# Optimization experiments

Measured on AMD Instinct MI355X. Metric: run time of the kernel, lower is better.

Reference implementation:

```python
import jax, jax.numpy as jnp
import numpy as np

T = 8192   # sequence length (sent_len)
D = 512    # word_emb_dim
H = 2048   # enc_lstm_dim
S = 512    # number of segments (len(action_pos))
EPS = 1e-4 # additive constant in the original _masked_softmax denominator


def setup_inputs() -> dict:
    key = jax.random.key(0)
    ks = jax.random.split(key, 16)
    s = 0.02  # small init scale keeps exp() stable
    seg_len = T // S
    action_pos = (jnp.arange(1, S + 1, dtype=jnp.int32) * seg_len - 1)  # last = T-1
    action = jnp.zeros((T,), jnp.int32).at[action_pos].set(1)
    return {
        "sent": jax.random.normal(ks[0], (T, D), jnp.float32),
        "Wi1": jax.random.normal(ks[1], (3 * H, D), jnp.float32) * s,
        "Wh1": jax.random.normal(ks[2], (3 * H, H), jnp.float32) * s,
        "bi1": jax.random.normal(ks[3], (3 * H,), jnp.float32) * s,
        "bh1": jax.random.normal(ks[4], (3 * H,), jnp.float32) * s,
        "Wi2": jax.random.normal(ks[5], (3 * H, H), jnp.float32) * s,
        "Wh2": jax.random.normal(ks[6], (3 * H, H), jnp.float32) * s,
        "bi2": jax.random.normal(ks[7], (3 * H,), jnp.float32) * s,
        "bh2": jax.random.normal(ks[8], (3 * H,), jnp.float32) * s,
        "Wl": jax.random.normal(ks[9], (H, H), jnp.float32) * s,
        "bl": jax.random.normal(ks[10], (H,), jnp.float32) * s,
        "wa": jax.random.normal(ks[11], (H,), jnp.float32) * s,
        "Wl2": jax.random.normal(ks[12], (H, H), jnp.float32) * s,
        "bl2": jax.random.normal(ks[13], (H,), jnp.float32) * s,
        "wa2": jax.random.normal(ks[14], (H,), jnp.float32) * s,
        "action": action,
        "action_pos": action_pos,
    }


def _gru_scan(xs, reset, Wi, Wh, bi, bh):
    """GRU over leading axis; hidden state zeroed after steps where reset==1.
    xs: (N, in), reset: (N,) int. Returns outputs (N, H)."""
    gi_all = xs @ Wi.T + bi  # (N, 3H) precompute input gates as one GEMM

    def step(h, inp):
        gi, a = inp
        gh = Wh @ h + bh
        r = jax.nn.sigmoid(gi[:H] + gh[:H])
        z = jax.nn.sigmoid(gi[H:2 * H] + gh[H:2 * H])
        n = jnp.tanh(gi[2 * H:] + r * gh[2 * H:])
        hn = (1.0 - z) * n + z * h
        h_next = jnp.where(a == 1, jnp.zeros_like(hn), hn)
        return h_next, hn

    h0 = jnp.zeros((H,), xs.dtype)
    _, outs = jax.lax.scan(step, h0, (gi_all, reset))
    return outs


def _degenerate_softmax(a):
    # Original sums exp over a size-1 axis: w = exp(a) / (exp(a) + 1e-4)
    e = jnp.exp(a)
    return e / (e + EPS)


def reference(sent, Wi1, Wh1, bi1, bh1, Wi2, Wh2, bi2, bh2,
              Wl, bl, wa, Wl2, bl2, wa2, action, action_pos):
    # lower GRU with per-step state reset
    outs = _gru_scan(sent, action, Wi1, Wh1, bi1, bh1)          # (T, H)
    emb_h = jnp.tanh(outs @ Wl.T + bl)                           # (T, H)
    w = _degenerate_softmax(emb_h @ wa)                          # (T,)
    weighted = w[:, None] * emb_h                                # (T, H)
    # segment i covers tokens (action_pos[i-1], action_pos[i]]
    seg_id = jnp.searchsorted(action_pos, jnp.arange(T), side='left')
    seg = jax.ops.segment_max(weighted, seg_id, num_segments=S)  # (S, H)
    # upper GRU over segment embeddings (no resets, zero init)
    outs2 = _gru_scan(seg, jnp.zeros((S,), jnp.int32), Wi2, Wh2, bi2, bh2)
    e2 = jnp.tanh(outs2 @ Wl2.T + bl2)                           # (S, H)
    w2 = _degenerate_softmax(e2 @ wa2)                           # (S,)
    emb = jnp.max(w2[:, None] * e2, axis=0, keepdims=True)       # (1, H)
    return emb
```

## Files before the change

### kernel.cpp

```cpp
#include <hip/hip_runtime.h>
#include <stdint.h>

typedef unsigned short u16;
typedef unsigned int u32;
typedef unsigned long long u64;
typedef __attribute__((ext_vector_type(4))) float f32x4;
typedef __attribute__((ext_vector_type(8))) short bf16x8;
typedef __attribute__((ext_vector_type(4))) u32 u32x4;

constexpr int kT = 8192;
constexpr int kD = 512;
constexpr int kH = 2048;
constexpr int kH3 = 6144;
constexpr int kS = 512;
constexpr int kSeg = 16;
constexpr int kNWG2 = 256;
constexpr int kREP = 4;

__device__ __forceinline__ float bf2f(u16 u) {
  union { float f; u32 u; } v; v.u = ((u32)u) << 16; return v.f;
}
__device__ __forceinline__ u16 f2bf(float f) {
  union { float f; u32 u; } v; v.f = f;
  u32 lsb = (v.u >> 16) & 1u;
  v.u += 0x7fffu + lsb;
  return (u16)(v.u >> 16);
}
__device__ __forceinline__ float bflo(u32 x) {
  union { float f; u32 u; } v; v.u = x << 16; return v.f;
}
__device__ __forceinline__ float bfhi(u32 x) {
  union { float f; u32 u; } v; v.u = x & 0xffff0000u; return v.f;
}
__device__ __forceinline__ float sigm(float x) { return 1.f / (1.f + expf(-x)); }

__device__ __forceinline__ void g2l16(const u16* g, u16* l) {
  __builtin_amdgcn_global_load_lds(
      (const __attribute__((address_space(1))) u32*)g,
      (__attribute__((address_space(3))) u32*)l, 16, 0, 0);
}

__device__ __forceinline__ u32x4 bypass_load16(const u32* p) {
  u32x4 v;
  asm volatile("global_load_dwordx4 %0, %1, off sc0 sc1\n\ts_waitcnt vmcnt(0)"
               : "=&v"(v) : "v"(p) : "memory");
  return v;
}
__device__ __forceinline__ void bypass_store4(u32* p, u32 v) {
  asm volatile("global_store_dword %0, %1, off sc0 sc1" :: "v"(p), "v"(v) : "memory");
}

struct Cvt7 {
  const float* s[7];
  u16* d[7];
  u32 pref[8];
};
__global__ __launch_bounds__(256) void cvt_all(Cvt7 j, int n4tot) {
  int i = blockIdx.x * 256 + threadIdx.x;
  if (i >= n4tot) return;
  int r = 0;
  while (i >= (int)j.pref[r + 1]) ++r;
  const int local = i - (int)j.pref[r];
  const float4 v = ((const float4*)j.s[r])[local];
  uint2 o;
  o.x = (u32)f2bf(v.x) | ((u32)f2bf(v.y) << 16);
  o.y = (u32)f2bf(v.z) | ((u32)f2bf(v.w) << 16);
  ((uint2*)j.d[r])[local] = o;
}

template<int EPI>
__global__ __launch_bounds__(256)
void gemm_bt(const u16* __restrict__ A, int lda,
             const u16* __restrict__ B, int ldb,
             u16* __restrict__ Obf, const float* __restrict__ bias,
             int M, int N, int K)
{
  __shared__ u16 ls[4 * 16384];
  const int tid = threadIdx.x;
  const int w = tid >> 6, lane = tid & 63;
  const int wr = w >> 1, wc = w & 1;
  const int arow0 = blockIdx.y * 128;
  const int brow0 = blockIdx.x * 128;
  const int srow = w * 32 + (lane >> 3);
  const int scol = (lane & 7) * 8;
  const u16* gA = A + (size_t)(arow0 + srow) * lda + scol;
  const u16* gB = B + (size_t)(brow0 + srow) * ldb + scol;
  const int sb = w * 32 * 64;

  f32x4 acc[4][4];
#pragma unroll
  for (int m = 0; m < 4; ++m)
#pragma unroll
    for (int n = 0; n < 4; ++n) acc[m][n] = (f32x4)0.f;

  const int fr = lane & 15;
  const int kq = lane >> 4;
  const int nk = K >> 6;

  auto stage = [&](int buf, int kt) {
    u16* la = &ls[buf * 16384 + sb];
    u16* lb = &ls[buf * 16384 + 8192 + sb];
#pragma unroll
    for (int i = 0; i < 4; ++i) g2l16(gA + (size_t)i * 8 * lda + kt, la + i * 8 * 64);
#pragma unroll
    for (int i = 0; i < 4; ++i) g2l16(gB + (size_t)i * 8 * ldb + kt, lb + i * 8 * 64);
  };

  stage(0, 0);
  if (nk > 1) stage(1, 64);
  if (nk > 2) stage(2, 128);

  for (int i = 0; i < nk; ++i) {
    if (i + 2 < nk) asm volatile("s_waitcnt vmcnt(16)" ::: "memory");
    else            asm volatile("s_waitcnt vmcnt(0)" ::: "memory");
    __builtin_amdgcn_s_barrier();
    __builtin_amdgcn_sched_barrier(0);
    if (i + 3 < nk) stage((i + 3) & 3, (i + 3) * 64);
    const u16* lsA = &ls[(i & 3) * 16384];
    const u16* lsB = lsA + 8192;
#pragma unroll
    for (int kk = 0; kk < 2; ++kk) {
      bf16x8 af[4], bq[4];
#pragma unroll
      for (int m = 0; m < 4; ++m)
        af[m] = *(const bf16x8*)&lsA[(wr * 64 + m * 16 + fr) * 64 + kk * 32 + kq * 8];
#pragma unroll
      for (int n = 0; n < 4; ++n)
        bq[n] = *(const bf16x8*)&lsB[(wc * 64 + n * 16 + fr) * 64 + kk * 32 + kq * 8];
#pragma unroll
      for (int m = 0; m < 4; ++m)
#pragma unroll
        for (int n = 0; n < 4; ++n)
          acc[m][n] = __builtin_amdgcn_mfma_f32_16x16x32_bf16(af[m], bq[n], acc[m][n], 0, 0, 0);
    }
  }

#pragma unroll
  for (int m = 0; m < 4; ++m) {
#pragma unroll
    for (int n = 0; n < 4; ++n) {
      const int row0 = arow0 + wr * 64 + m * 16 + kq * 4;
      const int col = brow0 + wc * 64 + n * 16 + fr;
      if (EPI == 1) {
#pragma unroll
        for (int i = 0; i < 4; ++i)
          Obf[(size_t)(row0 + i) * N + col] = f2bf(acc[m][n][i]);
      } else {
        const float bv = bias[col];
#pragma unroll
        for (int i = 0; i < 4; ++i)
          Obf[(size_t)(row0 + i) * N + col] = f2bf(tanhf(acc[m][n][i] + bv));
      }
    }
  }
}

template<int EPI>
__global__ __launch_bounds__(256)
void gemm_bt64(const u16* __restrict__ A, int lda,
               const u16* __restrict__ B, int ldb,
               u16* __restrict__ Obf, const float* __restrict__ bias,
               int M, int N, int K)
{
  __shared__ u16 ls[4 * 8192];
  const int tid = threadIdx.x;
  const int w = tid >> 6, lane = tid & 63;
  const int wr = w >> 1, wc = w & 1;
  const int arow0 = blockIdx.y * 64;
  const int brow0 = blockIdx.x * 64;
  const int srow = w * 16 + (lane >> 3);
  const int scol = (lane & 7) * 8;
  const u16* gA = A + (size_t)(arow0 + srow) * lda + scol;
  const u16* gB = B + (size_t)(brow0 + srow) * ldb + scol;
  const int sb = w * 16 * 64;

  f32x4 acc[2][2];
#pragma unroll
  for (int m = 0; m < 2; ++m)
#pragma unroll
    for (int n = 0; n < 2; ++n) acc[m][n] = (f32x4)0.f;

  const int fr = lane & 15;
  const int kq = lane >> 4;
  const int nk = K >> 6;

  auto stage = [&](int buf, int kt) {
    u16* la = &ls[buf * 8192 + sb];
    u16* lb = &ls[buf * 8192 + 4096 + sb];
#pragma unroll
    for (int i = 0; i < 2; ++i) g2l16(gA + (size_t)i * 8 * lda + kt, la + i * 8 * 64);
#pragma unroll
    for (int i = 0; i < 2; ++i) g2l16(gB + (size_t)i * 8 * ldb + kt, lb + i * 8 * 64);
  };

  stage(0, 0);
  if (nk > 1) stage(1, 64);
  if (nk > 2) stage(2, 128);

  for (int i = 0; i < nk; ++i) {
    if (i + 2 < nk) asm volatile("s_waitcnt vmcnt(8)" ::: "memory");
    else            asm volatile("s_waitcnt vmcnt(0)" ::: "memory");
    __builtin_amdgcn_s_barrier();
    __builtin_amdgcn_sched_barrier(0);
    if (i + 3 < nk) stage((i + 3) & 3, (i + 3) * 64);
    const u16* lsA = &ls[(i & 3) * 8192];
    const u16* lsB = lsA + 4096;
#pragma unroll
    for (int kk = 0; kk < 2; ++kk) {
      bf16x8 af[2], bq[2];
#pragma unroll
      for (int m = 0; m < 2; ++m)
        af[m] = *(const bf16x8*)&lsA[(wr * 32 + m * 16 + fr) * 64 + kk * 32 + kq * 8];
#pragma unroll
      for (int n = 0; n < 2; ++n)
        bq[n] = *(const bf16x8*)&lsB[(wc * 32 + n * 16 + fr) * 64 + kk * 32 + kq * 8];
#pragma unroll
      for (int m = 0; m < 2; ++m)
#pragma unroll
        for (int n = 0; n < 2; ++n)
          acc[m][n] = __builtin_amdgcn_mfma_f32_16x16x32_bf16(af[m], bq[n], acc[m][n], 0, 0, 0);
    }
  }

#pragma unroll
  for (int m = 0; m < 2; ++m) {
#pragma unroll
    for (int n = 0; n < 2; ++n) {
      const int row0 = arow0 + wr * 32 + m * 16 + kq * 4;
      const int col = brow0 + wc * 32 + n * 16 + fr;
      if (EPI == 1) {
#pragma unroll
        for (int i = 0; i < 4; ++i)
          Obf[(size_t)(row0 + i) * N + col] = f2bf(acc[m][n][i]);
      } else {
        const float bv = bias[col];
#pragma unroll
        for (int i = 0; i < 4; ++i)
          Obf[(size_t)(row0 + i) * N + col] = f2bf(tanhf(acc[m][n][i] + bv));
      }
    }
  }
}

__global__ __launch_bounds__(256) void gru1_gates(
    const u32* __restrict__ gi32, int segStride, const u16* __restrict__ gh,
    const float* __restrict__ bi, const float* __restrict__ bh,
    u16* __restrict__ h_bf, u16* __restrict__ outs_bf, int t, int ghvalid)
{
  const int idx = blockIdx.x * 256 + threadIdx.x;
  const int seg = idx >> 10, jp = idx & 1023;
  const u32* gh32 = (const u32*)gh;
  const int gbase = seg * segStride;
  const int base = seg * 3072;
  const u32 gir = gi32[gbase + jp];
  const u32 giz = gi32[gbase + 1024 + jp];
  const u32 gin = gi32[gbase + 2048 + jp];
  u32 ghr = 0, ghz = 0, ghn = 0, hp = 0;
  if (ghvalid) {
    ghr = gh32[base + jp];
    ghz = gh32[base + 1024 + jp];
    ghn = gh32[base + 2048 + jp];
    hp = ((const u32*)h_bf)[seg * 1024 + jp];
  }
  const float2 bir = *(const float2*)&bi[2 * jp];
  const float2 biz = *(const float2*)&bi[kH + 2 * jp];
  const float2 bin = *(const float2*)&bi[2 * kH + 2 * jp];
  const float2 bhr = *(const float2*)&bh[2 * jp];
  const float2 bhz = *(const float2*)&bh[kH + 2 * jp];
  const float2 bhn = *(const float2*)&bh[2 * kH + 2 * jp];
  float hn[2];
#pragma unroll
  for (int e = 0; e < 2; ++e) {
    const float gr = e ? bfhi(gir) : bflo(gir), hr = e ? bfhi(ghr) : bflo(ghr);
    const float gz = e ? bfhi(giz) : bflo(giz), hz = e ? bfhi(ghz) : bflo(ghz);
    const float gn = e ? bfhi(gin) : bflo(gin), hh = e ? bfhi(ghn) : bflo(ghn);
    const float r = sigm(gr + (e ? bir.y : bir.x) + hr + (e ? bhr.y : bhr.x));
    const float z = sigm(gz + (e ? biz.y : biz.x) + hz + (e ? bhz.y : bhz.x));
    const float n = tanhf(gn + (e ? bin.y : bin.x) + r * (hh + (e ? bhn.y : bhn.x)));
    const float hprev = e ? bfhi(hp) : bflo(hp);
    hn[e] = (1.f - z) * n + z * hprev;
  }
  const u32 packed = (u32)f2bf(hn[0]) | ((u32)f2bf(hn[1]) << 16);
  ((u32*)h_bf)[seg * 1024 + jp] = packed;
  ((u32*)outs_bf)[(size_t)(seg * kSeg + t) * 1024 + jp] = packed;
}

__global__ __launch_bounds__(256) void seg_weight_max(
    const u16* __restrict__ embh, const float* __restrict__ wa,
    u16* __restrict__ seg_bf)
{
  __shared__ float wrow[16];
  const int s = blockIdx.x, tid = threadIdx.x;
  const int w = tid >> 6, lane = tid & 63;
#pragma unroll
  for (int rr = 0; rr < 4; ++rr) {
    const int r = w * 4 + rr;
    const u16* row = embh + ((size_t)s * kSeg + r) * kH;
    float p = 0.f;
#pragma unroll
    for (int k = 0; k < 32; ++k) {
      const int c = lane + 64 * k;
      p += bf2f(row[c]) * wa[c];
    }
#pragma unroll
    for (int off = 32; off; off >>= 1) p += __shfl_down(p, off, 64);
    if (lane == 0) { const float e = expf(p); wrow[r] = e / (e + 1e-4f); }
  }
  __syncthreads();
#pragma unroll
  for (int i = 0; i < 8; ++i) {
    const int c = tid + 256 * i;
    float m = -1e30f;
#pragma unroll
    for (int r = 0; r < 16; ++r)
      m = fmaxf(m, wrow[r] * bf2f(embh[((size_t)s * kSeg + r) * kH + c]));
    seg_bf[(size_t)s * kH + c] = f2bf(m);
  }
}

__global__ __launch_bounds__(512)
void gru2_persistent(const u16* __restrict__ Wh2bf, const u16* __restrict__ gi2b,
                     const float* __restrict__ bi2, const float* __restrict__ bh2,
                     u32* __restrict__ hx,
                     u16* __restrict__ outs2)
{
  __shared__ u32 hlb[2][1024];
  __shared__ float gil_all[512 * 24];
  __shared__ u32 hnlt[8];
  const int wg = blockIdx.x, tid = threadIdx.x;
  const int g0 = wg * 8;
  const int rep = wg & (kREP - 1);
  const int w = tid >> 6, lane = tid & 63;
  const int jj = g0 + w;

  u32 wr_[16], wz_[16], wn_[16];
  {
    const u32* rr = (const u32*)(Wh2bf + (size_t)jj * kH);
    const u32* rz = (const u32*)(Wh2bf + (size_t)(kH + jj) * kH);
    const u32* rn = (const u32*)(Wh2bf + (size_t)(2 * kH + jj) * kH);
#pragma unroll
    for (int q = 0; q < 4; ++q)
#pragma unroll
      for (int i = 0; i < 4; ++i) {
        const int idx = q * 256 + lane * 4 + i;
        wr_[q * 4 + i] = rr[idx];
        wz_[q * 4 + i] = rz[idx];
        wn_[q * 4 + i] = rn[idx];
      }
  }
  for (int i = tid; i < 512 * 24; i += 512) {
    const int t = i / 24, idx = i - t * 24;
    gil_all[i] = bf2f(gi2b[(size_t)t * kH3 + (idx >> 3) * kH + g0 + (idx & 7)]);
  }
  const float bir = bi2[jj], biz = bi2[kH + jj], bin = bi2[2 * kH + jj];
  const float bhr = bh2[jj], bhz = bh2[kH + jj], bhn = bh2[2 * kH + jj];
  if (tid < 8) hnlt[tid] = 0;
  __syncthreads();

  for (int t = 0; t < 512; ++t) {
    const int par = t & 1;
    const u32 want = (u32)t & 0xffffu;
    const u32* p = hx + ((size_t)par * kREP + rep) * 2048 + 4 * tid;
    u32x4 v = bypass_load16(p);
    for (;;) {
      const u32 bad = ((v.x ^ want) | (v.y ^ want) | (v.z ^ want) | (v.w ^ want)) & 0xffffu;
      if (!__any((int)bad)) break;
      if (bad) v = bypass_load16(p);
    }
    hlb[par][2 * tid]     = (v.x >> 16) | (v.y & 0xffff0000u);
    hlb[par][2 * tid + 1] = (v.z >> 16) | (v.w & 0xffff0000u);
    __syncthreads();
    const uint4* hp4 = (const uint4*)&hlb[par][0];
    float ar = 0.f, az = 0.f, an = 0.f;
#pragma unroll
    for (int q = 0; q < 4; ++q) {
      const uint4 hv = hp4[q * 64 + lane];
      const float hf[8] = { bflo(hv.x), bfhi(hv.x), bflo(hv.y), bfhi(hv.y),
                            bflo(hv.z), bfhi(hv.z), bflo(hv.w), bfhi(hv.w) };
#pragma unroll
      for (int i = 0; i < 4; ++i) {
        const u32 wrv = wr_[q * 4 + i], wzv = wz_[q * 4 + i], wnv = wn_[q * 4 + i];
        ar += bflo(wrv) * hf[2 * i] + bfhi(wrv) * hf[2 * i + 1];
        az += bflo(wzv) * hf[2 * i] + bfhi(wzv) * hf[2 * i + 1];
        an += bflo(wnv) * hf[2 * i] + bfhi(wnv) * hf[2 * i + 1];
      }
    }
#pragma unroll
    for (int off = 32; off; off >>= 1) {
      ar += __shfl_down(ar, off, 64);
      az += __shfl_down(az, off, 64);
      an += __shfl_down(an, off, 64);
    }
    if (lane == 0) {
      const float r = sigm(gil_all[t * 24 + w] + bir + ar + bhr);
      const float z = sigm(gil_all[t * 24 + 8 + w] + biz + az + bhz);
      const float n = tanhf(gil_all[t * 24 + 16 + w] + bin + r * (an + bhn));
      const u32 hw = hlb[par][jj >> 1];
      const float hprev = (jj & 1) ? bfhi(hw) : bflo(hw);
      const u16 hb = f2bf((1.f - z) * n + z * hprev);
      const u32 word = ((u32)hb << 16) | ((u32)(t + 1) & 0xffffu);
      __hip_atomic_store(&hnlt[w], word, __ATOMIC_RELAXED, __HIP_MEMORY_SCOPE_WORKGROUP);
    }
    if (w == 0) {
      const u32 want1 = (u32)(t + 1) & 0xffffu;
      u32 x = 0;
      if (lane < 8) {
        for (;;) {
          x = __hip_atomic_load(&hnlt[lane], __ATOMIC_RELAXED, __HIP_MEMORY_SCOPE_WORKGROUP);
          if ((x & 0xffffu) == want1) break;
        }
      }
      const u32 word = __shfl(x, lane & 7, 64);
      if (lane < 4 * 8) {
        const int orep = lane >> 3;
        bypass_store4(hx + ((size_t)(1 - par) * kREP + orep) * 2048 + g0 + (lane & 7), word);
      }
      if (lane < 8) outs2[(size_t)t * kH + g0 + lane] = (u16)(x >> 16);
    }
  }
}

__global__ void calc_w2(const u16* __restrict__ e2, const float* __restrict__ wa2,
                        float* __restrict__ w2) {
  const int s = blockIdx.x, lane = threadIdx.x;
  float p = 0.f;
#pragma unroll
  for (int k = 0; k < 32; ++k) {
    const int c = lane + 64 * k;
    p += bf2f(e2[(size_t)s * kH + c]) * wa2[c];
  }
#pragma unroll
  for (int off = 32; off; off >>= 1) p += __shfl_down(p, off, 64);
  if (lane == 0) { const float e = expf(p); w2[s] = e / (e + 1e-4f); }
}

__global__ void final_max(const u16* __restrict__ e2, const float* __restrict__ w2,
                          float* __restrict__ out) {
  const int j = blockIdx.x * blockDim.x + threadIdx.x;
  float m = -1e30f;
  for (int s = 0; s < 512; ++s)
    m = fmaxf(m, w2[s] * bf2f(e2[(size_t)s * kH + j]));
  out[j] = m;
}

extern "C" void kernel_launch(void* const* d_in, const int* in_sizes, int n_in,
                              void* d_out, int out_size, void* d_ws, size_t ws_size,
                              hipStream_t stream)
{
  (void)in_sizes; (void)n_in; (void)out_size;
  const float* sent = (const float*)d_in[0];
  const float* Wi1f = (const float*)d_in[1];
  const float* Wh1f = (const float*)d_in[2];
  const float* bi1  = (const float*)d_in[3];
  const float* bh1  = (const float*)d_in[4];
  const float* Wi2f = (const float*)d_in[5];
  const float* Wh2f = (const float*)d_in[6];
  const float* bi2  = (const float*)d_in[7];
  const float* bh2  = (const float*)d_in[8];
  const float* Wlf  = (const float*)d_in[9];
  const float* bl   = (const float*)d_in[10];
  const float* wa   = (const float*)d_in[11];
  const float* Wl2f = (const float*)d_in[12];
  const float* bl2  = (const float*)d_in[13];
  const float* wa2  = (const float*)d_in[14];
  float* out = (float*)d_out;

  char* base = (char*)d_ws;
  size_t off = 0;
  auto alloc = [&](size_t b) { char* p = base + off; off += (b + 255) & ~(size_t)255; return p; };
  u16* sent_bf = (u16*)alloc((size_t)kT * kD * 2);
  u16* Wi1b    = (u16*)alloc((size_t)kH3 * kD * 2);
  u16* Wh1b    = (u16*)alloc((size_t)kH3 * kH * 2);
  u16* Wi2b    = (u16*)alloc((size_t)kH3 * kH * 2);
  u16* Wh2b    = (u16*)alloc((size_t)kH3 * kH * 2);
  u16* Wlb     = (u16*)alloc((size_t)kH * kH * 2);
  u16* Wl2b    = (u16*)alloc((size_t)kH * kH * 2);
  u16* gi_buf  = (u16*)alloc((size_t)kS * kH3 * 2);
  u16* gh_buf  = (u16*)alloc((size_t)kS * kH3 * 2);
  u16* h1b     = (u16*)alloc((size_t)kS * kH * 2);
  u16* outs_bf = (u16*)alloc((size_t)kT * kH * 2);
  u16* seg_bf  = (u16*)alloc((size_t)kS * kH * 2);
  u32* hx      = (u32*)alloc((size_t)2 * kREP * 2048 * 4);
  u16* outs2   = (u16*)alloc((size_t)kS * kH * 2);
  u16* e2b     = (u16*)alloc((size_t)kS * kH * 2);
  float* w2    = (float*)alloc(kS * 4);
  const size_t off_before_gi = off;
  u16* gi_all  = (u16*)alloc((size_t)kT * kH3 * 2);
  const bool fused_gi = (off <= ws_size);
  if (!fused_gi) off = off_before_gi;
  u16* embh = sent_bf;
  u16* gi2b = gi_buf;

  (void)hipMemsetAsync(hx, 0, (size_t)2 * kREP * 2048 * 4, stream);

  {
    Cvt7 j;
    const float* srcs[7] = { sent, Wi1f, Wh1f, Wi2f, Wh2f, Wlf, Wl2f };
    u16* dsts[7] = { sent_bf, Wi1b, Wh1b, Wi2b, Wh2b, Wlb, Wl2b };
    const u32 n4s[7] = { kT * kD / 4, kH3 * kD / 4, kH3 * kH / 4, kH3 * kH / 4,
                         kH3 * kH / 4, kH * kH / 4, kH * kH / 4 };
    u32 acc = 0;
    for (int r = 0; r < 7; ++r) { j.s[r] = srcs[r]; j.d[r] = dsts[r]; j.pref[r] = acc; acc += n4s[r]; }
    j.pref[7] = acc;
    cvt_all<<<dim3((acc + 255) / 256), dim3(256), 0, stream>>>(j, (int)acc);
  }

  if (fused_gi) {
    gemm_bt<1><<<dim3(kH3 / 128, kT / 128), dim3(256), 0, stream>>>(
        sent_bf, kD, Wi1b, kD, gi_all, nullptr, kT, kH3, kD);
  }
  for (int t = 0; t < kSeg; ++t) {
    if (t > 0) {
      gemm_bt64<1><<<dim3(kH3 / 64, kS / 64), dim3(256), 0, stream>>>(
          h1b, kH, Wh1b, kH, gh_buf, nullptr, kS, kH3, kH);
    }
    const u32* gi32;
    int segStride;
    if (fused_gi) {
      gi32 = (const u32*)gi_all + (size_t)t * 3072;
      segStride = kSeg * 3072;
    } else {
      gemm_bt64<1><<<dim3(kH3 / 64, kS / 64), dim3(256), 0, stream>>>(
          sent_bf + t * kD, kSeg * kD, Wi1b, kD, gi_buf, nullptr, kS, kH3, kD);
      gi32 = (const u32*)gi_buf;
      segStride = 3072;
    }
    gru1_gates<<<dim3(kS * kH / 512), dim3(256), 0, stream>>>(
        gi32, segStride, gh_buf, bi1, bh1, h1b, outs_bf, t, t > 0 ? 1 : 0);
  }
  gemm_bt<2><<<dim3(kH / 128, kT / 128), dim3(256), 0, stream>>>(
      outs_bf, kH, Wlb, kH, embh, bl, kT, kH, kH);
  seg_weight_max<<<dim3(kS), dim3(256), 0, stream>>>(embh, wa, seg_bf);
  gemm_bt64<1><<<dim3(kH3 / 64, kS / 64), dim3(256), 0, stream>>>(
      seg_bf, kH, Wi2b, kH, gi2b, nullptr, kS, kH3, kH);
  gru2_persistent<<<dim3(kNWG2), dim3(512), 0, stream>>>(
      Wh2b, gi2b, bi2, bh2, hx, outs2);
  gemm_bt64<2><<<dim3(kH / 64, kS / 64), dim3(256), 0, stream>>>(
      outs2, kH, Wl2b, kH, e2b, bl2, kS, kH, kH);
  calc_w2<<<dim3(kS), dim3(64), 0, stream>>>(e2b, wa2, w2);
  final_max<<<dim3(kH / 256), dim3(256), 0, stream>>>(e2b, w2, out);
}
```

Baseline: 2.566 ms.

## Fuse lower GRU recurrent GEMM with gate epilogue and double-buffer hidden state

Replaces the per-step recurrent GEMM plus separate gate kernel with one kernel that computes the r/z/n hidden projections for a 64-column slice across all three gates and applies the GRU update in its epilogue. This removes the gh_buf round trip and one launch per step. The hidden state is now ping-ponged between two buffers so the fused kernel can read the old state while writing the new one. A dedicated step-0 kernel skips the zero-state GEMM, and the remaining small GEMMs switch from the 64-tile to the 128-tile kernel. In exchange, the fused kernel launches only 256 blocks with larger LDS use (128 KB), and the switched small GEMMs get fewer blocks.

```diff
diff --git a/kernel.cpp b/kernel.cpp
--- a/kernel.cpp
+++ b/kernel.cpp
@@ -155,134 +155,118 @@
   }
 }
 
-template<int EPI>
 __global__ __launch_bounds__(256)
-void gemm_bt64(const u16* __restrict__ A, int lda,
-               const u16* __restrict__ B, int ldb,
-               u16* __restrict__ Obf, const float* __restrict__ bias,
-               int M, int N, int K)
+void gh_gates(const u16* __restrict__ h_in, const u16* __restrict__ Wh1b,
+              const u16* __restrict__ gi_p, int giStride,
+              const float* __restrict__ bi, const float* __restrict__ bh,
+              u16* __restrict__ h_out, u16* __restrict__ outs_p, int outsStride)
 {
-  __shared__ u16 ls[4 * 8192];
+  __shared__ u16 ls[4 * 16384];
   const int tid = threadIdx.x;
   const int w = tid >> 6, lane = tid & 63;
-  const int wr = w >> 1, wc = w & 1;
-  const int arow0 = blockIdx.y * 64;
-  const int brow0 = blockIdx.x * 64;
-  const int srow = w * 16 + (lane >> 3);
-  const int scol = (lane & 7) * 8;
-  const u16* gA = A + (size_t)(arow0 + srow) * lda + scol;
-  const u16* gB = B + (size_t)(brow0 + srow) * ldb + scol;
-  const int sb = w * 16 * 64;
-
-  f32x4 acc[2][2];
-#pragma unroll
-  for (int m = 0; m < 2; ++m)
-#pragma unroll
-    for (int n = 0; n < 2; ++n) acc[m][n] = (f32x4)0.f;
+  const int b = blockIdx.x;
+  const int xcd = b & 7, sub = (b >> 3) & 3, by = b >> 5;
+  const int bx = xcd * 4 + sub;
+  const int j0 = bx * 64, seg0 = by * 64;
+  const int srow = lane >> 3, scol = (lane & 7) * 8;
+  const u16* gA = h_in + (size_t)(seg0 + w * 16 + srow) * kH + scol;
+  const u16* gB[6];
+#pragma unroll
+  for (int i = 0; i < 6; ++i) {
+    const int lb = w * 48 + i * 8 + srow;
+    const int grow = (lb >> 6) * kH + j0 + (lb & 63);
+    gB[i] = Wh1b + (size_t)grow * kH + scol;
+  }
+  const int sbA = w * 16 * 64;
+  const int sbB = 4096 + w * 48 * 64;
+
+  f32x4 acc[12];
+#pragma unroll
+  for (int n = 0; n < 12; ++n) acc[n] = (f32x4)0.f;
 
   const int fr = lane & 15;
   const int kq = lane >> 4;
-  const int nk = K >> 6;
+  constexpr int nk = kH / 64;
 
   auto stage = [&](int buf, int kt) {
-    u16* la = &ls[buf * 8192 + sb];
-    u16* lb = &ls[buf * 8192 + 4096 + sb];
-#pragma unroll
-    for (int i = 0; i < 2; ++i) g2l16(gA + (size_t)i * 8 * lda + kt, la + i * 8 * 64);
-#pragma unroll
-    for (int i = 0; i < 2; ++i) g2l16(gB + (size_t)i * 8 * ldb + kt, lb + i * 8 * 64);
+    u16* base = &ls[buf * 16384];
+#pragma unroll
+    for (int i = 0; i < 2; ++i) g2l16(gA + (size_t)i * 8 * kH + kt, base + sbA + i * 8 * 64);
+#pragma unroll
+    for (int i = 0; i < 6; ++i) g2l16(gB[i] + kt, base + sbB + i * 8 * 64);
   };
 
   stage(0, 0);
-  if (nk > 1) stage(1, 64);
-  if (nk > 2) stage(2, 128);
+  stage(1, 64);
+  stage(2, 128);
 
   for (int i = 0; i < nk; ++i) {
-    if (i + 2 < nk) asm volatile("s_waitcnt vmcnt(8)" ::: "memory");
+    if (i + 2 < nk) asm volatile("s_waitcnt vmcnt(16)" ::: "memory");
     else            asm volatile("s_waitcnt vmcnt(0)" ::: "memory");
     __builtin_amdgcn_s_barrier();
     __builtin_amdgcn_sched_barrier(0);
     if (i + 3 < nk) stage((i + 3) & 3, (i + 3) * 64);
-    const u16* lsA = &ls[(i & 3) * 8192];
+    const u16* lsA = &ls[(i & 3) * 16384];
     const u16* lsB = lsA + 4096;
 #pragma unroll
     for (int kk = 0; kk < 2; ++kk) {
-      bf16x8 af[2], bq[2];
-#pragma unroll
-      for (int m = 0; m < 2; ++m)
-        af[m] = *(const bf16x8*)&lsA[(wr * 32 + m * 16 + fr) * 64 + kk * 32 + kq * 8];
-#pragma unroll
-      for (int n = 0; n < 2; ++n)
-        bq[n] = *(const bf16x8*)&lsB[(wc * 32 + n * 16 + fr) * 64 + kk * 32 + kq * 8];
-#pragma unroll
-      for (int m = 0; m < 2; ++m)
-#pragma unroll
-        for (int n = 0; n < 2; ++n)
-          acc[m][n] = __builtin_amdgcn_mfma_f32_16x16x32_bf16(af[m], bq[n], acc[m][n], 0, 0, 0);
-    }
-  }
-
-#pragma unroll
-  for (int m = 0; m < 2; ++m) {
-#pragma unroll
-    for (int n = 0; n < 2; ++n) {
-      const int row0 = arow0 + wr * 32 + m * 16 + kq * 4;
-      const int col = brow0 + wc * 32 + n * 16 + fr;
-      if (EPI == 1) {
-#pragma unroll
-        for (int i = 0; i < 4; ++i)
-          Obf[(size_t)(row0 + i) * N + col] = f2bf(acc[m][n][i]);
-      } else {
-        const float bv = bias[col];
-#pragma unroll
-        for (int i = 0; i < 4; ++i)
-          Obf[(size_t)(row0 + i) * N + col] = f2bf(tanhf(acc[m][n][i] + bv));
+      const bf16x8 af = *(const bf16x8*)&lsA[(w * 16 + fr) * 64 + kk * 32 + kq * 8];
+#pragma unroll
+      for (int n12 = 0; n12 < 12; ++n12) {
+        const bf16x8 bq = *(const bf16x8*)&lsB[(n12 * 16 + fr) * 64 + kk * 32 + kq * 8];
+        acc[n12] = __builtin_amdgcn_mfma_f32_16x16x32_bf16(af, bq, acc[n12], 0, 0, 0);
       }
     }
   }
-}
-
-__global__ __launch_bounds__(256) void gru1_gates(
-    const u32* __restrict__ gi32, int segStride, const u16* __restrict__ gh,
-    const float* __restrict__ bi, const float* __restrict__ bh,
-    u16* __restrict__ h_bf, u16* __restrict__ outs_bf, int t, int ghvalid)
+
+#pragma unroll
+  for (int n = 0; n < 4; ++n) {
+    const int jg = j0 + n * 16 + fr;
+    const float bir = bi[jg], biz = bi[kH + jg], bin = bi[2 * kH + jg];
+    const float bhr = bh[jg], bhz = bh[kH + jg], bhn = bh[2 * kH + jg];
+#pragma unroll
+    for (int ii = 0; ii < 4; ++ii) {
+      const int seg = seg0 + w * 16 + kq * 4 + ii;
+      const float ghr = acc[n][ii], ghz = acc[n + 4][ii], ghn = acc[n + 8][ii];
+      const size_t gio = (size_t)seg * giStride;
+      const float gir = bf2f(gi_p[gio + jg]);
+      const float giz = bf2f(gi_p[gio + kH + jg]);
+      const float gin = bf2f(gi_p[gio + 2 * kH + jg]);
+      const float r = sigm(gir + bir + ghr + bhr);
+      const float z = sigm(giz + biz + ghz + bhz);
+      const float nn = tanhf(gin + bin + r * (ghn + bhn));
+      const float hp = bf2f(h_in[(size_t)seg * kH + jg]);
+      const u16 hb = f2bf((1.f - z) * nn + z * hp);
+      h_out[(size_t)seg * kH + jg] = hb;
+      outs_p[(size_t)seg * outsStride + jg] = hb;
+    }
+  }
+}
+
+__global__ __launch_bounds__(256) void gru1_gates0(
+    const u32* __restrict__ gi32, int segStride,
+    const float* __restrict__ bi,
+    u16* __restrict__ h_bf, u16* __restrict__ outs_bf)
 {
   const int idx = blockIdx.x * 256 + threadIdx.x;
   const int seg = idx >> 10, jp = idx & 1023;
-  const u32* gh32 = (const u32*)gh;
   const int gbase = seg * segStride;
-  const int base = seg * 3072;
-  const u32 gir = gi32[gbase + jp];
   const u32 giz = gi32[gbase + 1024 + jp];
   const u32 gin = gi32[gbase + 2048 + jp];
-  u32 ghr = 0, ghz = 0, ghn = 0, hp = 0;
-  if (ghvalid) {
-    ghr = gh32[base + jp];
-    ghz = gh32[base + 1024 + jp];
-    ghn = gh32[base + 2048 + jp];
-    hp = ((const u32*)h_bf)[seg * 1024 + jp];
-  }
-  const float2 bir = *(const float2*)&bi[2 * jp];
   const float2 biz = *(const float2*)&bi[kH + 2 * jp];
   const float2 bin = *(const float2*)&bi[2 * kH + 2 * jp];
-  const float2 bhr = *(const float2*)&bh[2 * jp];
-  const float2 bhz = *(const float2*)&bh[kH + 2 * jp];
-  const float2 bhn = *(const float2*)&bh[2 * kH + 2 * jp];
   float hn[2];
 #pragma unroll
   for (int e = 0; e < 2; ++e) {
-    const float gr = e ? bfhi(gir) : bflo(gir), hr = e ? bfhi(ghr) : bflo(ghr);
-    const float gz = e ? bfhi(giz) : bflo(giz), hz = e ? bfhi(ghz) : bflo(ghz);
-    const float gn = e ? bfhi(gin) : bflo(gin), hh = e ? bfhi(ghn) : bflo(ghn);
-    const float r = sigm(gr + (e ? bir.y : bir.x) + hr + (e ? bhr.y : bhr.x));
-    const float z = sigm(gz + (e ? biz.y : biz.x) + hz + (e ? bhz.y : bhz.x));
-    const float n = tanhf(gn + (e ? bin.y : bin.x) + r * (hh + (e ? bhn.y : bhn.x)));
-    const float hprev = e ? bfhi(hp) : bflo(hp);
-    hn[e] = (1.f - z) * n + z * hprev;
+    const float gz = e ? bfhi(giz) : bflo(giz);
+    const float gn = e ? bfhi(gin) : bflo(gin);
+    const float z = sigm(gz + (e ? biz.y : biz.x));
+    const float n = tanhf(gn + (e ? bin.y : bin.x));
+    hn[e] = (1.f - z) * n;
   }
   const u32 packed = (u32)f2bf(hn[0]) | ((u32)f2bf(hn[1]) << 16);
   ((u32*)h_bf)[seg * 1024 + jp] = packed;
-  ((u32*)outs_bf)[(size_t)(seg * kSeg + t) * 1024 + jp] = packed;
+  ((u32*)outs_bf)[(size_t)(seg * kSeg) * 1024 + jp] = packed;
 }
 
 __global__ __launch_bounds__(256) void seg_weight_max(
@@ -476,8 +460,8 @@
   u16* Wlb     = (u16*)alloc((size_t)kH * kH * 2);
   u16* Wl2b    = (u16*)alloc((size_t)kH * kH * 2);
   u16* gi_buf  = (u16*)alloc((size_t)kS * kH3 * 2);
-  u16* gh_buf  = (u16*)alloc((size_t)kS * kH3 * 2);
-  u16* h1b     = (u16*)alloc((size_t)kS * kH * 2);
+  u16* h1a     = (u16*)alloc((size_t)kS * kH * 2);
+  u16* h1c     = (u16*)alloc((size_t)kS * kH * 2);
   u16* outs_bf = (u16*)alloc((size_t)kT * kH * 2);
   u16* seg_bf  = (u16*)alloc((size_t)kS * kH * 2);
   u32* hx      = (u32*)alloc((size_t)2 * kREP * 2048 * 4);
@@ -509,33 +493,38 @@
     gemm_bt<1><<<dim3(kH3 / 128, kT / 128), dim3(256), 0, stream>>>(
         sent_bf, kD, Wi1b, kD, gi_all, nullptr, kT, kH3, kD);
   }
+  u16* h_cur = h1a;
+  u16* h_nxt = h1c;
   for (int t = 0; t < kSeg; ++t) {
-    if (t > 0) {
-      gemm_bt64<1><<<dim3(kH3 / 64, kS / 64), dim3(256), 0, stream>>>(
-          h1b, kH, Wh1b, kH, gh_buf, nullptr, kS, kH3, kH);
-    }
-    const u32* gi32;
-    int segStride;
+    const u16* gi_p;
+    int giStride;
     if (fused_gi) {
-      gi32 = (const u32*)gi_all + (size_t)t * 3072;
-      segStride = kSeg * 3072;
+      gi_p = gi_all + (size_t)t * kH3;
+      giStride = kSeg * kH3;
     } else {
-      gemm_bt64<1><<<dim3(kH3 / 64, kS / 64), dim3(256), 0, stream>>>(
+      gemm_bt<1><<<dim3(kH3 / 128, kS / 128), dim3(256), 0, stream>>>(
           sent_bf + t * kD, kSeg * kD, Wi1b, kD, gi_buf, nullptr, kS, kH3, kD);
-      gi32 = (const u32*)gi_buf;
-      segStride = 3072;
-    }
-    gru1_gates<<<dim3(kS * kH / 512), dim3(256), 0, stream>>>(
-        gi32, segStride, gh_buf, bi1, bh1, h1b, outs_bf, t, t > 0 ? 1 : 0);
+      gi_p = gi_buf;
+      giStride = kH3;
+    }
+    if (t == 0) {
+      gru1_gates0<<<dim3(kS * kH / 512), dim3(256), 0, stream>>>(
+          (const u32*)gi_p, giStride / 2, bi1, h_cur, outs_bf);
+    } else {
+      gh_gates<<<dim3(256), dim3(256), 0, stream>>>(
+          h_cur, Wh1b, gi_p, giStride, bi1, bh1,
+          h_nxt, outs_bf + (size_t)t * kH, kSeg * kH);
+      u16* tmp = h_cur; h_cur = h_nxt; h_nxt = tmp;
+    }
   }
   gemm_bt<2><<<dim3(kH / 128, kT / 128), dim3(256), 0, stream>>>(
       outs_bf, kH, Wlb, kH, embh, bl, kT, kH, kH);
   seg_weight_max<<<dim3(kS), dim3(256), 0, stream>>>(embh, wa, seg_bf);
-  gemm_bt64<1><<<dim3(kH3 / 64, kS / 64), dim3(256), 0, stream>>>(
+  gemm_bt<1><<<dim3(kH3 / 128, kS / 128), dim3(256), 0, stream>>>(
       seg_bf, kH, Wi2b, kH, gi2b, nullptr, kS, kH3, kH);
   gru2_persistent<<<dim3(kNWG2), dim3(512), 0, stream>>>(
       Wh2b, gi2b, bi2, bh2, hx, outs2);
-  gemm_bt64<2><<<dim3(kH / 64, kS / 64), dim3(256), 0, stream>>>(
+  gemm_bt<2><<<dim3(kH / 128, kS / 128), dim3(256), 0, stream>>>(
       outs2, kH, Wl2b, kH, e2b, bl2, kS, kH, kH);
   calc_w2<<<dim3(kS), dim3(64), 0, stream>>>(e2b, wa2, w2);
   final_max<<<dim3(kH / 256), dim3(256), 0, stream>>>(e2b, w2, out);
```

Measured after the change: 2.578 ms. About the same (+0.5%).
